# Kernel tuning notes

Hardware: AMD Instinct MI355X
Metric: run time of the kernel (lower is better)

## Reference

```python
import jax, jax.numpy as jnp
import numpy as np

STRIDE = (1, 1)
PADDING = ((1, 1), (1, 1))


def setup_inputs() -> dict:
    key = jax.random.key(0)
    k1, k2 = jax.random.split(key)
    x = jax.random.normal(k1, (32, 256, 56, 56), dtype=jnp.float32)
    # kaiming-uniform-like init scale (matches _ConvNd.reset_parameters magnitude roughly)
    fan_in = 256 * 3 * 3
    bound = float(np.sqrt(1.0 / fan_in))
    weight = jax.random.uniform(k2, (256, 256, 3, 3), dtype=jnp.float32,
                                minval=-bound, maxval=bound)
    return {"x": x, "weight": weight}


def reference(x, weight):
    # per-output-filter mean of |w| over (in_ch, kh, kw)
    a = jnp.mean(jnp.abs(weight), axis=(1, 2, 3), keepdims=True)  # [O,1,1,1]
    b = jnp.sign(weight)
    binary_weight = b * a
    out = jax.lax.conv_general_dilated(
        x, binary_weight,
        window_strides=STRIDE,
        padding=PADDING,
        dimension_numbers=("NCHW", "OIHW", "NCHW"),
    )
    return out
```

## Files before the change

kernel.cpp:

```cpp
#include <hip/hip_runtime.h>
#include <cstdint>
#include <cstddef>

#define WB_OFF   55115776ull
#define AL_OFF   (WB_OFF + 1179648ull)

typedef __bf16 bf16x8 __attribute__((ext_vector_type(8)));
typedef float  f32x4  __attribute__((ext_vector_type(4)));

static __device__ __forceinline__ unsigned short f2bf(float f) {
  union { float f; unsigned int u; } v; v.f = f;
  unsigned int u = v.u;
  u += 0x7FFFu + ((u >> 16) & 1u);
  return (unsigned short)(u >> 16);
}

static __device__ __forceinline__ void async16(void* lds, const void* g) {
  __builtin_amdgcn_global_load_lds(
      (const __attribute__((address_space(1))) unsigned int*)g,
      (__attribute__((address_space(3))) unsigned int*)lds, 16, 0, 0);
}

__global__ void prep_w(const float* __restrict__ w, unsigned short* __restrict__ wb,
                       float* __restrict__ alpha) {
  const int o = blockIdx.x, c = threadIdx.x;
  const float* wr = w + (size_t)(o * 256 + c) * 9;
  float s = 0.f;
#pragma unroll
  for (int tap = 0; tap < 9; ++tap) {
    float v = wr[tap];
    s += fabsf(v);
    unsigned short sg = (v > 0.f) ? 0x3F80u : ((v < 0.f) ? 0xBF80u : 0u);
    wb[(size_t)o * 2304 + tap * 256 + c] = sg;
  }
  __shared__ float red[256];
  red[c] = s;
  __syncthreads();
  for (int d = 128; d > 0; d >>= 1) {
    if (c < d) red[c] += red[c + d];
    __syncthreads();
  }
  if (c == 0) alpha[o] = red[0] * (1.f / 2304.f);
}

__global__ __launch_bounds__(256) void prep_x(const float* __restrict__ x,
                                              unsigned short* __restrict__ xp) {
  const int bx = blockIdx.x;
  const int n = bx / 58, hp = bx % 58;
  const int t = threadIdx.x;
  unsigned short* row = xp + (size_t)(n * 58 + hp) * 58 * 256;

  if (hp == 0 || hp == 57) {
    uint32_t* r32 = (uint32_t*)row;
    for (int i = t; i < 7424; i += 256) r32[i] = 0;
    return;
  }
  const int h = hp - 1;
  __shared__ unsigned short tile[56 * 258];

  const int w = t & 63, cw = t >> 6;
  if (w < 56) {
    const float* src = x + ((size_t)(n * 256 + cw) * 56 + h) * 56 + w;
#pragma unroll 8
    for (int k = 0; k < 64; ++k) {
      tile[w * 258 + (k * 4 + cw)] = f2bf(*src);
      src += (size_t)4 * 3136;
    }
  }
  __syncthreads();

  uint32_t* r32 = (uint32_t*)row;
  if (t < 128) { r32[t] = 0; r32[57 * 128 + t] = 0; }
#pragma unroll
  for (int it = 0; it < 28; ++it) {
    const int id = it * 256 + t;
    const int ww = id >> 7, cp = id & 127;
    const uint32_t lo = tile[ww * 258 + 2 * cp];
    const uint32_t hi = tile[ww * 258 + 2 * cp + 1];
    r32[(ww + 1) * 128 + cp] = lo | (hi << 16);
  }
}

__global__ __launch_bounds__(256, 4)
void conv_mfma(const unsigned short* __restrict__ xp,
               const unsigned short* __restrict__ wb,
               const float* __restrict__ alpha,
               float* __restrict__ out) {
  __shared__ __align__(16) char lds[32768];
  char* ldsA = lds;
  char* ldsB = lds + 16384;

  const int tid = threadIdx.x;
  const int wave = tid >> 6, lane = tid & 63;
  const int wm = wave >> 1, wn = wave & 1;
  const int o0 = (blockIdx.x >= 784) ? 128 : 0;
  const int pix0 = (blockIdx.x % 784) * 128;

  const int rsub = lane >> 3;
  const int schunk = (lane & 7) ^ rsub;

  const char* gA[4];
  const char* gB[4];
#pragma unroll
  for (int j = 0; j < 4; ++j) {
    const int row = (wave * 4 + j) * 8 + rsub;
    gA[j] = (const char*)wb + (size_t)(o0 + row) * 4608 + schunk * 16;
    const int pix = pix0 + row;
    const int n = pix / 3136, rem = pix % 3136;
    const int h = rem / 56, ww = rem % 56;
    gB[j] = (const char*)xp + (size_t)((n * 58 + h) * 58 + ww) * 512 + schunk * 16;
  }

  f32x4 acc[4][4];
#pragma unroll
  for (int i = 0; i < 4; ++i)
#pragma unroll
    for (int j = 0; j < 4; ++j) acc[i][j] = (f32x4){0.f, 0.f, 0.f, 0.f};

  const int ar = lane & 15, aq = lane >> 4;
  const int sw = ar & 7;

  for (int tap = 0; tap < 9; ++tap) {
    const int tapoff = ((tap / 3) * 58 + (tap % 3)) * 512;
#pragma unroll
    for (int cc = 0; cc < 4; ++cc) {
      const int kA = tap * 512 + cc * 128;
      const int kB = tapoff + cc * 128;
      __syncthreads();
#pragma unroll
      for (int j = 0; j < 4; ++j) {
        async16(ldsA + (wave * 4 + j) * 1024, gA[j] + kA);
        async16(ldsB + (wave * 4 + j) * 1024, gB[j] + kB);
      }
      __syncthreads();
#pragma unroll
      for (int kk = 0; kk < 2; ++kk) {
        bf16x8 af[4], bfr[4];
#pragma unroll
        for (int mi = 0; mi < 4; ++mi)
          af[mi] = *(const bf16x8*)(ldsA + (wm * 64 + mi * 16 + ar) * 128 +
                                    (((kk * 4 + aq) ^ sw) * 16));
#pragma unroll
        for (int ni = 0; ni < 4; ++ni)
          bfr[ni] = *(const bf16x8*)(ldsB + (wn * 64 + ni * 16 + ar) * 128 +
                                     (((kk * 4 + aq) ^ sw) * 16));
#pragma unroll
        for (int mi = 0; mi < 4; ++mi)
#pragma unroll
          for (int ni = 0; ni < 4; ++ni)
            acc[mi][ni] = __builtin_amdgcn_mfma_f32_16x16x32_bf16(af[mi], bfr[ni],
                                                                  acc[mi][ni], 0, 0, 0);
      }
    }
  }

  int nc[4], rc[4];
#pragma unroll
  for (int ni = 0; ni < 4; ++ni) {
    const int pix = pix0 + wn * 64 + ni * 16 + ar;
    nc[ni] = pix / 3136; rc[ni] = pix % 3136;
  }
#pragma unroll
  for (int mi = 0; mi < 4; ++mi) {
    const int orow = o0 + wm * 64 + mi * 16 + aq * 4;
    float al[4];
#pragma unroll
    for (int r = 0; r < 4; ++r) al[r] = alpha[orow + r];
#pragma unroll
    for (int ni = 0; ni < 4; ++ni) {
      const size_t base = (size_t)nc[ni] * 802816 + (size_t)orow * 3136 + (size_t)rc[ni];
#pragma unroll
      for (int r = 0; r < 4; ++r)
        out[base + (size_t)r * 3136] = acc[mi][ni][r] * al[r];
    }
  }
}

extern "C" void kernel_launch(void* const* d_in, const int* in_sizes, int n_in,
                              void* d_out, int out_size, void* d_ws, size_t ws_size,
                              hipStream_t stream) {
  const float* x = (const float*)d_in[0];
  const float* w = (const float*)d_in[1];
  char* ws = (char*)d_ws;
  unsigned short* xp  = (unsigned short*)ws;
  unsigned short* wbp = (unsigned short*)(ws + WB_OFF);
  float* alpha = (float*)(ws + AL_OFF);
  float* out = (float*)d_out;

  prep_w<<<256, 256, 0, stream>>>(w, wbp, alpha);
  prep_x<<<32 * 58, 256, 0, stream>>>(x, xp);
  conv_mfma<<<1568, 256, 0, stream>>>(xp, wbp, alpha, out);
}
```

Measured before the change: 357.1 us.

## Double-buffer input tiles in LDS and load weight fragments directly to registers

The conv GEMM loop now keeps only the input (B) tile in LDS. It is double-buffered, with the next K-step prefetched via global_load_lds while the current one is consumed, which cuts the barriers per step from two to one. Weight (A) fragments are read straight from global/L2 into registers, so they no longer pass through LDS. Launch bounds drop from 4 to 3 blocks per CU to allow more registers for the extra A fragments. The trade-offs are exposed global latency on the weight loads, less coalesced weight access, and possibly lower occupancy.

```diff
diff --git a/kernel.cpp b/kernel.cpp
--- a/kernel.cpp
+++ b/kernel.cpp
@@ -81,14 +81,12 @@
   }
 }
 
-__global__ __launch_bounds__(256, 4)
+__global__ __launch_bounds__(256, 3)
 void conv_mfma(const unsigned short* __restrict__ xp,
                const unsigned short* __restrict__ wb,
                const float* __restrict__ alpha,
                float* __restrict__ out) {
   __shared__ __align__(16) char lds[32768];
-  char* ldsA = lds;
-  char* ldsB = lds + 16384;
 
   const int tid = threadIdx.x;
   const int wave = tid >> 6, lane = tid & 63;
@@ -98,57 +96,71 @@
 
   const int rsub = lane >> 3;
   const int schunk = (lane & 7) ^ rsub;
-
-  const char* gA[4];
+  const int ar = lane & 15, aq = lane >> 4;
+  const int sw = ar & 7;
+
   const char* gB[4];
 #pragma unroll
   for (int j = 0; j < 4; ++j) {
-    const int row = (wave * 4 + j) * 8 + rsub;
-    gA[j] = (const char*)wb + (size_t)(o0 + row) * 4608 + schunk * 16;
-    const int pix = pix0 + row;
+    const int pix = pix0 + (wave * 4 + j) * 8 + rsub;
     const int n = pix / 3136, rem = pix % 3136;
     const int h = rem / 56, ww = rem % 56;
     gB[j] = (const char*)xp + (size_t)((n * 58 + h) * 58 + ww) * 512 + schunk * 16;
   }
 
+  const char* gAf[4];
+#pragma unroll
+  for (int mi = 0; mi < 4; ++mi)
+    gAf[mi] = (const char*)wb + (size_t)(o0 + wm * 64 + mi * 16 + ar) * 4608 + aq * 16;
+
   f32x4 acc[4][4];
 #pragma unroll
   for (int i = 0; i < 4; ++i)
 #pragma unroll
     for (int j = 0; j < 4; ++j) acc[i][j] = (f32x4){0.f, 0.f, 0.f, 0.f};
 
-  const int ar = lane & 15, aq = lane >> 4;
-  const int sw = ar & 7;
+#pragma unroll
+  for (int j = 0; j < 4; ++j)
+    async16(lds + (wave * 4 + j) * 1024, gB[j]);
 
   for (int tap = 0; tap < 9; ++tap) {
     const int tapoff = ((tap / 3) * 58 + (tap % 3)) * 512;
+    const int ntapoff = (tap < 8) ? (((tap + 1) / 3) * 58 + ((tap + 1) % 3)) * 512 : 0;
 #pragma unroll
     for (int cc = 0; cc < 4; ++cc) {
+      const int step = tap * 4 + cc;
+      char* bufc = lds + (cc & 1) * 16384;
+      char* bufn = lds + ((cc & 1) ^ 1) * 16384;
+
+      __syncthreads();
+
       const int kA = tap * 512 + cc * 128;
-      const int kB = tapoff + cc * 128;
-      __syncthreads();
-#pragma unroll
-      for (int j = 0; j < 4; ++j) {
-        async16(ldsA + (wave * 4 + j) * 1024, gA[j] + kA);
-        async16(ldsB + (wave * 4 + j) * 1024, gB[j] + kB);
+      bf16x8 af[2][4];
+#pragma unroll
+      for (int kk = 0; kk < 2; ++kk)
+#pragma unroll
+        for (int mi = 0; mi < 4; ++mi)
+          af[kk][mi] = *(const bf16x8*)(gAf[mi] + (kA + kk * 64));
+
+      if (step + 1 < 36) {
+        const int kBn = (cc < 3) ? (tapoff + (cc + 1) * 128) : ntapoff;
+#pragma unroll
+        for (int j = 0; j < 4; ++j)
+          async16(bufn + (wave * 4 + j) * 1024, gB[j] + kBn);
       }
-      __syncthreads();
+
 #pragma unroll
       for (int kk = 0; kk < 2; ++kk) {
-        bf16x8 af[4], bfr[4];
+        bf16x8 bfr[4];
+#pragma unroll
+        for (int ni = 0; ni < 4; ++ni)
+          bfr[ni] = *(const bf16x8*)(bufc + (wn * 64 + ni * 16 + ar) * 128 +
+                                     (((kk * 4 + aq) ^ sw) * 16));
 #pragma unroll
         for (int mi = 0; mi < 4; ++mi)
-          af[mi] = *(const bf16x8*)(ldsA + (wm * 64 + mi * 16 + ar) * 128 +
-                                    (((kk * 4 + aq) ^ sw) * 16));
-#pragma unroll
-        for (int ni = 0; ni < 4; ++ni)
-          bfr[ni] = *(const bf16x8*)(ldsB + (wn * 64 + ni * 16 + ar) * 128 +
-                                     (((kk * 4 + aq) ^ sw) * 16));
-#pragma unroll
-        for (int mi = 0; mi < 4; ++mi)
 #pragma unroll
           for (int ni = 0; ni < 4; ++ni)
-            acc[mi][ni] = __builtin_amdgcn_mfma_f32_16x16x32_bf16(af[mi], bfr[ni],
+            acc[mi][ni] = __builtin_amdgcn_mfma_f32_16x16x32_bf16(af[kk][mi], bfr[ni],
                                                                   acc[mi][ni], 0, 0, 0);
       }
     }
```

New measurement: 492.5 us. 37.9% more time.

## Switch conv GEMM to 32x32x16 MFMA with two-wave 256x128 block tiles

Applied to the files above, without the earlier changes.

Replaces the 16x16x32 bf16 MFMA with the 32x32x16 variant and restructures the block to two waves covering all 256 output channels by 128 pixels, with 128x128 per-wave tiles and 16-register accumulators. The input pixel tile is loaded once per block for all output channels rather than twice across two channel-half blocks, which cuts global and LDS traffic per MFMA. In exchange, each block has only 128 threads, uses 48KB of LDS and a large accumulator set (256 floats per lane), so occupancy drops sharply and latency hiding around the per-step barriers gets worse. The epilogue is rewritten to the 32x32 output register layout.

```diff
diff --git a/kernel.cpp b/kernel.cpp
--- a/kernel.cpp
+++ b/kernel.cpp
@@ -6,7 +6,7 @@
 #define AL_OFF   (WB_OFF + 1179648ull)
 
 typedef __bf16 bf16x8 __attribute__((ext_vector_type(8)));
-typedef float  f32x4  __attribute__((ext_vector_type(4)));
+typedef float  f32x16 __attribute__((ext_vector_type(16)));
 
 static __device__ __forceinline__ unsigned short f2bf(float f) {
   union { float f; unsigned int u; } v; v.f = f;
@@ -81,44 +81,41 @@
   }
 }
 
-__global__ __launch_bounds__(256, 4)
+__global__ __launch_bounds__(128, 1)
 void conv_mfma(const unsigned short* __restrict__ xp,
                const unsigned short* __restrict__ wb,
                const float* __restrict__ alpha,
                float* __restrict__ out) {
-  __shared__ __align__(16) char lds[32768];
+  __shared__ __align__(16) char lds[49152];
   char* ldsA = lds;
-  char* ldsB = lds + 16384;
+  char* ldsB = lds + 32768;
 
   const int tid = threadIdx.x;
   const int wave = tid >> 6, lane = tid & 63;
-  const int wm = wave >> 1, wn = wave & 1;
-  const int o0 = (blockIdx.x >= 784) ? 128 : 0;
-  const int pix0 = (blockIdx.x % 784) * 128;
+  const int pix0 = blockIdx.x * 128;
 
   const int rsub = lane >> 3;
   const int schunk = (lane & 7) ^ rsub;
+  const int l31 = lane & 31, half = lane >> 5, sw7 = lane & 7;
 
-  const char* gA[4];
-  const char* gB[4];
+  const char* gA = (const char*)wb + (size_t)(wave * 128 + rsub) * 4608 + schunk * 16;
+
+  const char* gB[8];
 #pragma unroll
-  for (int j = 0; j < 4; ++j) {
-    const int row = (wave * 4 + j) * 8 + rsub;
-    gA[j] = (const char*)wb + (size_t)(o0 + row) * 4608 + schunk * 16;
-    const int pix = pix0 + row;
+  for (int j = 0; j < 8; ++j) {
+    const int pix = pix0 + wave * 64 + j * 8 + rsub;
     const int n = pix / 3136, rem = pix % 3136;
     const int h = rem / 56, ww = rem % 56;
     gB[j] = (const char*)xp + (size_t)((n * 58 + h) * 58 + ww) * 512 + schunk * 16;
   }
 
-  f32x4 acc[4][4];
+  f32x16 acc[4][4];
 #pragma unroll
   for (int i = 0; i < 4; ++i)
 #pragma unroll
-    for (int j = 0; j < 4; ++j) acc[i][j] = (f32x4){0.f, 0.f, 0.f, 0.f};
-
-  const int ar = lane & 15, aq = lane >> 4;
-  const int sw = ar & 7;
+    for (int j = 0; j < 4; ++j)
+#pragma unroll
+      for (int e = 0; e < 16; ++e) acc[i][j][e] = 0.f;
 
   for (int tap = 0; tap < 9; ++tap) {
     const int tapoff = ((tap / 3) * 58 + (tap % 3)) * 512;
@@ -128,50 +125,49 @@
       const int kB = tapoff + cc * 128;
       __syncthreads();
 #pragma unroll
-      for (int j = 0; j < 4; ++j) {
-        async16(ldsA + (wave * 4 + j) * 1024, gA[j] + kA);
-        async16(ldsB + (wave * 4 + j) * 1024, gB[j] + kB);
-      }
+      for (int j = 0; j < 16; ++j)
+        async16(ldsA + wave * 16384 + j * 1024, gA + (size_t)j * 8 * 4608 + kA);
+#pragma unroll
+      for (int j = 0; j < 8; ++j)
+        async16(ldsB + wave * 8192 + j * 1024, gB[j] + kB);
       __syncthreads();
+
 #pragma unroll
-      for (int kk = 0; kk < 2; ++kk) {
+      for (int kk = 0; kk < 4; ++kk) {
+        const int ch = ((kk * 2 + half) ^ sw7) * 16;
         bf16x8 af[4], bfr[4];
 #pragma unroll
         for (int mi = 0; mi < 4; ++mi)
-          af[mi] = *(const bf16x8*)(ldsA + (wm * 64 + mi * 16 + ar) * 128 +
-                                    (((kk * 4 + aq) ^ sw) * 16));
+          af[mi] = *(const bf16x8*)(ldsA + (wave * 128 + mi * 32 + l31) * 128 + ch);
 #pragma unroll
         for (int ni = 0; ni < 4; ++ni)
-          bfr[ni] = *(const bf16x8*)(ldsB + (wn * 64 + ni * 16 + ar) * 128 +
-                                     (((kk * 4 + aq) ^ sw) * 16));
+          bfr[ni] = *(const bf16x8*)(ldsB + (ni * 32 + l31) * 128 + ch);
 #pragma unroll
         for (int mi = 0; mi < 4; ++mi)
 #pragma unroll
           for (int ni = 0; ni < 4; ++ni)
-            acc[mi][ni] = __builtin_amdgcn_mfma_f32_16x16x32_bf16(af[mi], bfr[ni],
+            acc[mi][ni] = __builtin_amdgcn_mfma_f32_32x32x16_bf16(af[mi], bfr[ni],
                                                                   acc[mi][ni], 0, 0, 0);
       }
     }
   }
 
-  int nc[4], rc[4];
+  int nn[4], rr[4];
 #pragma unroll
   for (int ni = 0; ni < 4; ++ni) {
-    const int pix = pix0 + wn * 64 + ni * 16 + ar;
-    nc[ni] = pix / 3136; rc[ni] = pix % 3136;
+    const int pix = pix0 + ni * 32 + l31;
+    nn[ni] = pix / 3136; rr[ni] = pix % 3136;
   }
 #pragma unroll
   for (int mi = 0; mi < 4; ++mi) {
-    const int orow = o0 + wm * 64 + mi * 16 + aq * 4;
-    float al[4];
 #pragma unroll
-    for (int r = 0; r < 4; ++r) al[r] = alpha[orow + r];
+    for (int reg = 0; reg < 16; ++reg) {
+      const int o = wave * 128 + mi * 32 + (reg & 3) + 8 * (reg >> 2) + 4 * half;
+      const float a = alpha[o];
+      const size_t obase = (size_t)o * 3136;
 #pragma unroll
-    for (int ni = 0; ni < 4; ++ni) {
-      const size_t base = (size_t)nc[ni] * 802816 + (size_t)orow * 3136 + (size_t)rc[ni];
-#pragma unroll
-      for (int r = 0; r < 4; ++r)
-        out[base + (size_t)r * 3136] = acc[mi][ni][r] * al[r];
+      for (int ni = 0; ni < 4; ++ni)
+        out[(size_t)nn[ni] * 802816 + obase + (size_t)rr[ni]] = acc[mi][ni][reg] * a;
     }
   }
 }
@@ -189,5 +185,5 @@
 
   prep_w<<<256, 256, 0, stream>>>(w, wbp, alpha);
   prep_x<<<32 * 58, 256, 0, stream>>>(x, xp);
-  conv_mfma<<<1568, 256, 0, stream>>>(xp, wbp, alpha, out);
+  conv_mfma<<<784, 128, 0, stream>>>(xp, wbp, alpha, out);
 }
```

Result: slower. 401.4 us (+12.4%).
